# Kernel optimization log

Hardware: AMD Instinct MI355X
Metric: run time of the kernel (lower is better)

The kernel has to match this reference:

```python
import jax, jax.numpy as jnp
import numpy as np

N, E, IN_DIM, HID, HEADS, OUT_DIM, N_GRAPHS = 50000, 640000, 128, 64, 8, 2, 64
NEG_SLOPE = 0.2  # PyG GATConv default leaky_relu slope


def setup_inputs() -> dict:
    key = jax.random.key(0)
    ks = jax.random.split(key, 12)
    x = jax.random.normal(ks[0], (N, IN_DIM), jnp.float32)
    edge_index = jax.random.randint(ks[1], (2, E), 0, N, jnp.int32)
    batch = jnp.sort(jax.random.randint(ks[2], (N,), 0, N_GRAPHS, jnp.int32))
    def glorot(k, shape):
        fan_in = shape[0]
        return jax.random.normal(k, shape, jnp.float32) / np.sqrt(fan_in)
    return {
        "x": x,
        "W1": glorot(ks[3], (IN_DIM, HEADS * HID)),
        "att_src1": glorot(ks[4], (HEADS, HID)),
        "att_dst1": glorot(ks[5], (HEADS, HID)),
        "b1": jnp.zeros((HEADS * HID,), jnp.float32),
        "W2": glorot(ks[6], (HEADS * HID, HID)),
        "att_src2": glorot(ks[7], (1, HID)),
        "att_dst2": glorot(ks[8], (1, HID)),
        "b2": jnp.zeros((HID,), jnp.float32),
        "fc_w": glorot(ks[9], (HID, OUT_DIM)),
        "fc_b": jnp.zeros((OUT_DIM,), jnp.float32),
        "edge_index": edge_index,
        "batch": batch,
    }


def gat_layer(x, src, dst, W, a_src, a_dst, bias):
    # PyG GATConv: h = x @ W per head; alpha_e = LeakyReLU(a_src.h_src + a_dst.h_dst),
    # softmax over edges sharing the same dst, weighted scatter-sum, concat heads.
    H, C = a_src.shape
    h = (x @ W).reshape(-1, H, C)                       # [N, H, C]
    a_s = jnp.einsum('nhc,hc->nh', h, a_src)            # [N, H]
    a_d = jnp.einsum('nhc,hc->nh', h, a_dst)
    e = jax.nn.leaky_relu(a_s[src] + a_d[dst], NEG_SLOPE)  # [Etot, H]
    e_max = jax.ops.segment_max(e, dst, num_segments=N)
    e = jnp.exp(e - e_max[dst])
    denom = jax.ops.segment_sum(e, dst, num_segments=N)
    alpha = e / (denom[dst] + 1e-16)                    # edge softmax
    msg = h[src] * alpha[..., None]                     # [Etot, H, C]
    out = jax.ops.segment_sum(msg, dst, num_segments=N) # [N, H, C]
    return out.reshape(-1, H * C) + bias


def reference(x, W1, att_src1, att_dst1, b1, W2, att_src2, att_dst2, b2, fc_w, fc_b, edge_index, batch):
    # add self-loops (PyG GATConv default add_self_loops=True)
    loop = jnp.arange(N, dtype=edge_index.dtype)
    src = jnp.concatenate([edge_index[0], loop])
    dst = jnp.concatenate([edge_index[1], loop])

    h = gat_layer(x, src, dst, W1, att_src1, att_dst1, b1)   # [N, HEADS*HID]
    h = jax.nn.elu(h)
    # dropout is identity at eval
    h = gat_layer(h, src, dst, W2, att_src2, att_dst2, b2)   # [N, HID]
    h = jax.nn.elu(h)

    # global mean pool over graphs
    sums = jax.ops.segment_sum(h, batch, num_segments=N_GRAPHS)
    cnts = jax.ops.segment_sum(jnp.ones((N, 1), h.dtype), batch, num_segments=N_GRAPHS)
    pooled = sums / jnp.maximum(cnts, 1.0)                   # [G, HID]
    return pooled @ fc_w + fc_b                              # [G, OUT_DIM]
```

## Files before the change

### kernel.cpp

```cpp
#include <hip/hip_runtime.h>
#include <hip/hip_bf16.h>
#include <cstdint>
#include <cstddef>

#define N_NODES   50000
#define N_EDGES   640000
#define ETOT      (N_EDGES + N_NODES)
#define IN_DIM    128
#define HID       64
#define HEADS     8
#define F1        (HEADS * HID)
#define OUT_DIM   2
#define N_GRAPHS  64
#define NEG_SLOPE 0.2f
#define CAP       64

typedef __attribute__((ext_vector_type(8))) short s8v;
typedef __attribute__((ext_vector_type(4))) float f32x4;
typedef __attribute__((ext_vector_type(2))) float f32x2;
typedef unsigned char uchar;
typedef unsigned int  uint;
typedef unsigned long long u64;

__device__ __forceinline__ float leakyf(float x) { return x > 0.f ? x : NEG_SLOPE * x; }
__device__ __forceinline__ float eluf(float x)   { return x > 0.f ? x : __expf(x) - 1.f; }

__device__ __forceinline__ ushort f2bf(float f) {
    union { float f; uint32_t i; } c; c.f = f;
    uint32_t r = c.i + 0x7FFFu + ((c.i >> 16) & 1u);
    return (ushort)(r >> 16);
}
template<int SEL>
__device__ __forceinline__ float fp8f(uint w) {
    return __builtin_amdgcn_cvt_f32_fp8(w, SEL);
}
template<bool HI>
__device__ __forceinline__ f32x2 pk8(uint w) {
    return __builtin_amdgcn_cvt_pk_f32_fp8(w, HI);
}
__device__ __forceinline__ int orig64(int q) { return ((q & 3) << 4) | (q >> 2); }

#define W1_ITEMS  (F1 * IN_DIM)
#define W2_ITEMS  (HID * F1)
#define PM_ITEMS  (F1 + HID + HID * OUT_DIM)
#define PREP_ITEMS (ETOT + W1_ITEMS + W2_ITEMS + PM_ITEMS)

__global__ __launch_bounds__(256) void prep_fill(const int* __restrict__ srcI,
                                                 const int* __restrict__ dstI,
                                                 int* __restrict__ counts,
                                                 ushort* __restrict__ csrp,
                                                 const float* __restrict__ W1,
                                                 const float* __restrict__ W2,
                                                 const float* __restrict__ b1,
                                                 const float* __restrict__ b2,
                                                 const float* __restrict__ fcw,
                                                 ushort* __restrict__ W1T,
                                                 ushort* __restrict__ W2T,
                                                 float* __restrict__ b1p,
                                                 float* __restrict__ b2p,
                                                 float* __restrict__ fcwp) {
    int i = blockIdx.x * 256 + threadIdx.x;
    if (i < ETOT) {
        int s, d;
        if (i < N_EDGES) { s = srcI[i]; d = dstI[i]; }
        else             { s = d = i - N_EDGES; }
        int slot = atomicAdd(&counts[d], 1);
        if (slot < CAP) csrp[d * CAP + slot] = (ushort)s;
    } else if (i < ETOT + W1_ITEMS) {
        int idx = i - ETOT;
        int n = idx >> 7, k = idx & 127;
        W1T[idx] = f2bf(W1[(size_t)k * F1 + n]);
    } else if (i < ETOT + W1_ITEMS + W2_ITEMS) {
        int idx = i - ETOT - W1_ITEMS;
        int n = idx >> 9, kp = idx & 511;
        int ko = (kp & 448) | orig64(kp & 63);
        W2T[idx] = f2bf(W2[(size_t)ko * HID + n]);
    } else if (i < PREP_ITEMS) {
        int j = i - ETOT - W1_ITEMS - W2_ITEMS;
        if (j < F1) {
            b1p[j] = b1[(j & ~63) | orig64(j & 63)];
        } else if (j < F1 + HID) {
            int q = j - F1;
            b2p[q] = b2[orig64(q)];
        } else {
            int q = j - F1 - HID;
            int ch = q >> 1, o = q & 1;
            fcwp[q] = fcw[orig64(ch) * OUT_DIM + o];
        }
    }
}

template<int BM, int BN, int BK, int AH, bool AF32>
__global__ __launch_bounds__(256) void gemm_att(const void* __restrict__ Av,
                                                const ushort* __restrict__ BT,
                                                uchar* __restrict__ C8,
                                                int M, int N, int K,
                                                const float* __restrict__ att_s,
                                                const float* __restrict__ att_d,
                                                float* __restrict__ as_o,
                                                float* __restrict__ ad_o) {
    int nwg = gridDim.x;
    int q = nwg >> 3, r = nwg & 7;
    int xcd = blockIdx.x & 7, loc = blockIdx.x >> 3;
    int sid = (xcd < r) ? (xcd * (q + 1) + loc)
                        : (r * (q + 1) + (xcd - r) * q + loc);
    int ncb = N / BN;
    int bx = sid % ncb;
    int by = sid / ncb;

    __shared__ ushort As[BM * BK];
    __shared__ ushort Bs[BN * BK];
    const int t    = threadIdx.x;
    const int row0 = by * BM;
    const int col0 = bx * BN;
    const int lane = t & 63;
    const int wr   = t >> 6;
    constexpr int FR = BM / 64;

    f32x4 acc[FR][4];
    #pragma unroll
    for (int i = 0; i < FR; ++i)
        #pragma unroll
        for (int j = 0; j < 4; ++j)
            acc[i][j] = (f32x4){0.f, 0.f, 0.f, 0.f};

    constexpr int A_IT = BM * BK / 8 / 256;
    constexpr int B_IT = BN * BK / 8 / 256;

    for (int k0 = 0; k0 < K; k0 += BK) {
        #pragma unroll
        for (int i = 0; i < A_IT; ++i) {
            int ch  = t + 256 * i;
            int rr  = ch >> 3;
            int c16 = ch & 7;
            int gr = row0 + rr;
            uint4 v = make_uint4(0u, 0u, 0u, 0u);
            if constexpr (AF32) {
                const float* Af = (const float*)Av;
                if (gr < M) {
                    const float* pr = Af + (size_t)gr * K + k0 + c16 * 8;
                    float4 f0 = *reinterpret_cast<const float4*>(pr);
                    float4 f1 = *reinterpret_cast<const float4*>(pr + 4);
                    v.x = ((uint)f2bf(f0.y) << 16) | f2bf(f0.x);
                    v.y = ((uint)f2bf(f0.w) << 16) | f2bf(f0.z);
                    v.z = ((uint)f2bf(f1.y) << 16) | f2bf(f1.x);
                    v.w = ((uint)f2bf(f1.w) << 16) | f2bf(f1.z);
                }
            } else {
                const ushort* Ab = (const ushort*)Av;
                if (gr < M)
                    v = *reinterpret_cast<const uint4*>(Ab + (size_t)gr * K + k0 + c16 * 8);
            }
            int off = (ch * 16) ^ ((rr & 7) << 4);
            *reinterpret_cast<uint4*>(reinterpret_cast<char*>(As) + off) = v;
        }
        #pragma unroll
        for (int i = 0; i < B_IT; ++i) {
            int ch  = t + 256 * i;
            int rr  = ch >> 3;
            int c16 = ch & 7;
            uint4 v = *reinterpret_cast<const uint4*>(BT + (size_t)(col0 + rr) * K + k0 + c16 * 8);
            int off = (ch * 16) ^ ((rr & 7) << 4);
            *reinterpret_cast<uint4*>(reinterpret_cast<char*>(Bs) + off) = v;
        }
        __syncthreads();
        #pragma unroll
        for (int kk = 0; kk < BK; kk += 32) {
            s8v af[FR], bf[4];
            #pragma unroll
            for (int fr = 0; fr < FR; ++fr) {
                int rr  = wr * (FR * 16) + fr * 16 + (lane & 15);
                int off = (rr * (BK * 2) + kk * 2 + (lane >> 4) * 16) ^ ((rr & 7) << 4);
                af[fr] = *reinterpret_cast<const s8v*>(reinterpret_cast<const char*>(As) + off);
            }
            #pragma unroll
            for (int fc = 0; fc < 4; ++fc) {
                int rr  = fc * 16 + (lane & 15);
                int off = (rr * (BK * 2) + kk * 2 + (lane >> 4) * 16) ^ ((rr & 7) << 4);
                bf[fc] = *reinterpret_cast<const s8v*>(reinterpret_cast<const char*>(Bs) + off);
            }
            #pragma unroll
            for (int fr = 0; fr < FR; ++fr)
                #pragma unroll
                for (int fc = 0; fc < 4; ++fc)
                    acc[fr][fc] = __builtin_amdgcn_mfma_f32_16x16x32_bf16(af[fr], bf[fc], acc[fr][fc], 0, 0, 0);
        }
        __syncthreads();
    }

    float avs[4], avd[4];
    const float* asp = att_s + bx * BN;
    const float* adp = att_d + bx * BN;
    #pragma unroll
    for (int fc = 0; fc < 4; ++fc) {
        avs[fc] = asp[fc * 16 + (lane & 15)];
        avd[fc] = adp[fc * 16 + (lane & 15)];
    }

    #pragma unroll
    for (int fr = 0; fr < FR; ++fr) {
        #pragma unroll
        for (int j = 0; j < 4; ++j) {
            int row = row0 + wr * (FR * 16) + fr * 16 + (lane >> 4) * 4 + j;
            if (row < M) {
                uint pk = __builtin_amdgcn_cvt_pk_fp8_f32(acc[fr][0][j], acc[fr][1][j], 0u, false);
                pk = __builtin_amdgcn_cvt_pk_fp8_f32(acc[fr][2][j], acc[fr][3][j], pk, true);
                *reinterpret_cast<uint*>(C8 + (size_t)row * N + col0 + (lane & 15) * 4) = pk;
                float sv = 0.f, dv = 0.f;
                #pragma unroll
                for (int fc = 0; fc < 4; ++fc) {
                    float c = acc[fr][fc][j];
                    sv = fmaf(c, avs[fc], sv);
                    dv = fmaf(c, avd[fc], dv);
                }
                #pragma unroll
                for (int off = 1; off < 16; off <<= 1) {
                    sv += __shfl_xor(sv, off);
                    dv += __shfl_xor(dv, off);
                }
                if ((lane & 15) == 0) {
                    as_o[(size_t)row * AH + bx] = sv;
                    ad_o[(size_t)row * AH + bx] = dv;
                }
            }
        }
    }
}

__global__ __launch_bounds__(256) void gat_agg1(const uchar* __restrict__ h8,
                                                const float* __restrict__ as,
                                                const float* __restrict__ ad,
                                                const int* __restrict__ counts,
                                                const ushort* __restrict__ csrp,
                                                const float* __restrict__ b1p,
                                                ushort* __restrict__ z) {
    __shared__ float lds_w[4][HEADS][CAP + 1];
    int tid  = threadIdx.x;
    int wid  = tid >> 6;
    int dst  = (blockIdx.x * 256 + tid) >> 6;
    int lane = tid & 63;
    if (dst >= N_NODES) return;
    int cnt = min(counts[dst], CAP);
    int hd  = lane >> 3;

    int myidx = (lane < cnt) ? (int)csrp[(size_t)dst * CAP + lane] : 0;
    float4 a0 = *reinterpret_cast<const float4*>(as + (size_t)myidx * HEADS);
    float4 a1 = *reinterpret_cast<const float4*>(as + (size_t)myidx * HEADS + 4);
    float4 d0 = *reinterpret_cast<const float4*>(ad + (size_t)dst * HEADS);
    float4 d1 = *reinterpret_cast<const float4*>(ad + (size_t)dst * HEADS + 4);
    lds_w[wid][0][lane] = __expf(leakyf(a0.x + d0.x));
    lds_w[wid][1][lane] = __expf(leakyf(a0.y + d0.y));
    lds_w[wid][2][lane] = __expf(leakyf(a0.z + d0.z));
    lds_w[wid][3][lane] = __expf(leakyf(a0.w + d0.w));
    lds_w[wid][4][lane] = __expf(leakyf(a1.x + d1.x));
    lds_w[wid][5][lane] = __expf(leakyf(a1.y + d1.y));
    lds_w[wid][6][lane] = __expf(leakyf(a1.z + d1.z));
    lds_w[wid][7][lane] = __expf(leakyf(a1.w + d1.w));

    f32x2 acc2[4];
    acc2[0] = (f32x2){0.f, 0.f}; acc2[1] = (f32x2){0.f, 0.f};
    acc2[2] = (f32x2){0.f, 0.f}; acc2[3] = (f32x2){0.f, 0.f};
    float den = 0.f;
    const uchar* hb = h8 + (size_t)lane * 8;
    for (int j0 = 0; j0 < cnt; j0 += 4) {
        int n = cnt - j0;
        int s0 = 0, s1 = 0, s2 = 0, s3 = 0;
        u64 v0 = 0, v1 = 0, v2 = 0, v3 = 0;
        float w0 = 0.f, w1 = 0.f, w2 = 0.f, w3 = 0.f;
        s0 = __shfl(myidx, j0);
        v0 = __builtin_nontemporal_load(reinterpret_cast<const u64*>(hb + (size_t)s0 * F1));
        w0 = lds_w[wid][hd][j0];
        if (n > 1) {
            s1 = __shfl(myidx, j0 + 1);
            v1 = __builtin_nontemporal_load(reinterpret_cast<const u64*>(hb + (size_t)s1 * F1));
            w1 = lds_w[wid][hd][j0 + 1];
        }
        if (n > 2) {
            s2 = __shfl(myidx, j0 + 2);
            v2 = __builtin_nontemporal_load(reinterpret_cast<const u64*>(hb + (size_t)s2 * F1));
            w2 = lds_w[wid][hd][j0 + 2];
        }
        if (n > 3) {
            s3 = __shfl(myidx, j0 + 3);
            v3 = __builtin_nontemporal_load(reinterpret_cast<const u64*>(hb + (size_t)s3 * F1));
            w3 = lds_w[wid][hd][j0 + 3];
        }
        {
            f32x2 wv = (f32x2){w0, w0};
            den += w0;
            acc2[0] += pk8<false>((uint)v0) * wv;
            acc2[1] += pk8<true >((uint)v0) * wv;
            acc2[2] += pk8<false>((uint)(v0 >> 32)) * wv;
            acc2[3] += pk8<true >((uint)(v0 >> 32)) * wv;
        }
        if (n > 1) {
            f32x2 wv = (f32x2){w1, w1};
            den += w1;
            acc2[0] += pk8<false>((uint)v1) * wv;
            acc2[1] += pk8<true >((uint)v1) * wv;
            acc2[2] += pk8<false>((uint)(v1 >> 32)) * wv;
            acc2[3] += pk8<true >((uint)(v1 >> 32)) * wv;
        }
        if (n > 2) {
            f32x2 wv = (f32x2){w2, w2};
            den += w2;
            acc2[0] += pk8<false>((uint)v2) * wv;
            acc2[1] += pk8<true >((uint)v2) * wv;
            acc2[2] += pk8<false>((uint)(v2 >> 32)) * wv;
            acc2[3] += pk8<true >((uint)(v2 >> 32)) * wv;
        }
        if (n > 3) {
            f32x2 wv = (f32x2){w3, w3};
            den += w3;
            acc2[0] += pk8<false>((uint)v3) * wv;
            acc2[1] += pk8<true >((uint)v3) * wv;
            acc2[2] += pk8<false>((uint)(v3 >> 32)) * wv;
            acc2[3] += pk8<true >((uint)(v3 >> 32)) * wv;
        }
    }
    float inv = 1.f / (den + 1e-16f);
    s8v ov;
    #pragma unroll
    for (int c = 0; c < 8; ++c) {
        float v = acc2[c >> 1][c & 1] * inv + b1p[lane * 8 + c];
        ov[c] = (short)f2bf(eluf(v));
    }
    *reinterpret_cast<s8v*>(z + (size_t)dst * F1 + lane * 8) = ov;
}

__global__ __launch_bounds__(256) void gat_agg2(const uchar* __restrict__ h8,
                                                const float* __restrict__ as,
                                                const float* __restrict__ ad,
                                                const int* __restrict__ counts,
                                                const ushort* __restrict__ csrp,
                                                const float* __restrict__ b2p,
                                                float* __restrict__ z) {
    int dst  = (blockIdx.x * 256 + threadIdx.x) >> 6;
    int lane = threadIdx.x & 63;
    if (dst >= N_NODES) return;
    int cnt = min(counts[dst], CAP);
    float adv = ad[dst];

    int myidx = (lane < cnt) ? (int)csrp[(size_t)dst * CAP + lane] : 0;
    float wl  = (lane < cnt) ? __expf(leakyf(as[myidx] + adv)) : 0.f;
    float den = wl;
    #pragma unroll
    for (int off = 32; off > 0; off >>= 1) den += __shfl_xor(den, off);

    float acc = 0.f;
    for (int j0 = 0; j0 < cnt; j0 += 4) {
        int n = cnt - j0;
        int s0 = 0, s1 = 0, s2 = 0, s3 = 0;
        float w0 = 0.f, w1 = 0.f, w2 = 0.f, w3 = 0.f;
        uint b0 = 0, b1 = 0, b2 = 0, b3 = 0;
        s0 = __shfl(myidx, j0);     w0 = __shfl(wl, j0);
        b0 = h8[(size_t)s0 * HID + lane];
        if (n > 1) { s1 = __shfl(myidx, j0 + 1); w1 = __shfl(wl, j0 + 1); b1 = h8[(size_t)s1 * HID + lane]; }
        if (n > 2) { s2 = __shfl(myidx, j0 + 2); w2 = __shfl(wl, j0 + 2); b2 = h8[(size_t)s2 * HID + lane]; }
        if (n > 3) { s3 = __shfl(myidx, j0 + 3); w3 = __shfl(wl, j0 + 3); b3 = h8[(size_t)s3 * HID + lane]; }
        acc = fmaf(w0, fp8f<0>(b0), acc);
        if (n > 1) acc = fmaf(w1, fp8f<0>(b1), acc);
        if (n > 2) acc = fmaf(w2, fp8f<0>(b2), acc);
        if (n > 3) acc = fmaf(w3, fp8f<0>(b3), acc);
    }
    float v = acc / (den + 1e-16f) + b2p[lane];
    z[(size_t)dst * HID + lane] = eluf(v);
}

__global__ __launch_bounds__(512) void pool_fc(const float* __restrict__ z,
                                               const int* __restrict__ batch,
                                               const float* __restrict__ fcwp,
                                               const float* __restrict__ fc_b,
                                               float* __restrict__ out) {
    int g = blockIdx.x;
    int t = threadIdx.x, lane = t & 63, w = t >> 6;
    auto lb = [&](int key) {
        int lo = 0, hi = N_NODES;
        while (lo < hi) { int mid = (lo + hi) >> 1; if (batch[mid] < key) lo = mid + 1; else hi = mid; }
        return lo;
    };
    int lo = lb(g), hi = lb(g + 1);
    float a0 = 0.f, a1 = 0.f, a2 = 0.f, a3 = 0.f;
    for (int n0 = lo + (w << 2); n0 < hi; n0 += 32) {
        a0 += z[(size_t)n0 * HID + lane];
        if (n0 + 1 < hi) a1 += z[(size_t)(n0 + 1) * HID + lane];
        if (n0 + 2 < hi) a2 += z[(size_t)(n0 + 2) * HID + lane];
        if (n0 + 3 < hi) a3 += z[(size_t)(n0 + 3) * HID + lane];
    }
    float acc = (a0 + a1) + (a2 + a3);
    __shared__ float sh[8][HID];
    sh[w][lane] = acc;
    __syncthreads();
    if (w == 0) {
        float s = 0.f;
        #pragma unroll
        for (int i = 0; i < 8; ++i) s += sh[i][lane];
        float cntf = fmaxf((float)(hi - lo), 1.f);
        float mean = s / cntf;
        float p0 = mean * fcwp[lane * OUT_DIM + 0];
        float p1 = mean * fcwp[lane * OUT_DIM + 1];
        #pragma unroll
        for (int off = 32; off > 0; off >>= 1) {
            p0 += __shfl_xor(p0, off);
            p1 += __shfl_xor(p1, off);
        }
        if (lane == 0) {
            out[g * OUT_DIM + 0] = p0 + fc_b[0];
            out[g * OUT_DIM + 1] = p1 + fc_b[1];
        }
    }
}

extern "C" void kernel_launch(void* const* d_in, const int* in_sizes, int n_in,
                              void* d_out, int out_size, void* d_ws, size_t ws_size,
                              hipStream_t stream) {
    const float* x    = (const float*)d_in[0];
    const float* W1   = (const float*)d_in[1];
    const float* at_s1= (const float*)d_in[2];
    const float* at_d1= (const float*)d_in[3];
    const float* b1   = (const float*)d_in[4];
    const float* W2   = (const float*)d_in[5];
    const float* at_s2= (const float*)d_in[6];
    const float* at_d2= (const float*)d_in[7];
    const float* b2   = (const float*)d_in[8];
    const float* fcw  = (const float*)d_in[9];
    const float* fcb  = (const float*)d_in[10];
    const int*   ei   = (const int*)d_in[11];
    const int*   batch= (const int*)d_in[12];
    float* out = (float*)d_out;

    char* p = (char*)d_ws;
    auto alloc = [&](size_t bytes) {
        char* r = p;
        p += (bytes + 255) & ~size_t(255);
        return r;
    };
    int*    counts= (int*)alloc((size_t)N_NODES * 4);
    ushort* W1T   = (ushort*)alloc((size_t)F1 * IN_DIM * 2);
    ushort* W2T   = (ushort*)alloc((size_t)HID * F1 * 2);
    float*  b1p   = (float*)alloc((size_t)F1 * 4);
    float*  b2p   = (float*)alloc((size_t)HID * 4);
    float*  fcwp  = (float*)alloc((size_t)HID * OUT_DIM * 4);
    uchar*  h1    = (uchar*)alloc((size_t)N_NODES * F1);
    ushort* z1    = (ushort*)alloc((size_t)N_NODES * F1 * 2);
    uchar*  h2    = (uchar*)alloc((size_t)N_NODES * HID);
    float*  z2    = (float*)alloc((size_t)N_NODES * HID * 4);
    float*  as1   = (float*)alloc((size_t)N_NODES * HEADS * 4);
    float*  ad1   = (float*)alloc((size_t)N_NODES * HEADS * 4);
    float*  as2   = (float*)alloc((size_t)N_NODES * 4);
    float*  ad2   = (float*)alloc((size_t)N_NODES * 4);
    ushort* csrp  = (ushort*)alloc((size_t)N_NODES * CAP * 2);

    const int* srcI = ei;
    const int* dstI = ei + N_EDGES;

    (void)hipMemsetAsync(counts, 0, (size_t)N_NODES * 4, stream);

    prep_fill<<<(PREP_ITEMS + 255) / 256, 256, 0, stream>>>(
        srcI, dstI, counts, csrp, W1, W2, b1, b2, fcw, W1T, W2T, b1p, b2p, fcwp);

    int nwg1 = (F1 / 64) * ((N_NODES + 127) / 128);
    gemm_att<128, 64, 64, HEADS, true><<<nwg1, 256, 0, stream>>>(
        x, W1T, h1, N_NODES, F1, IN_DIM, at_s1, at_d1, as1, ad1);
    gat_agg1<<<(N_NODES + 3) / 4, 256, 0, stream>>>(h1, as1, ad1, counts, csrp, b1p, z1);

    int nwg2 = 1 * ((N_NODES + 127) / 128);
    gemm_att<128, 64, 64, 1, false><<<nwg2, 256, 0, stream>>>(
        z1, W2T, h2, N_NODES, HID, F1, at_s2, at_d2, as2, ad2);
    gat_agg2<<<(N_NODES + 3) / 4, 256, 0, stream>>>(h2, as2, ad2, counts, csrp, b2p, z2);

    pool_fc<<<N_GRAPHS, 512, 0, stream>>>(z2, batch, fcwp, fcb, out);
}
```

Measured before the change: 308.5 us.

## Fuse mean-pool into second aggregation via atomics; retile layer-2 GEMM; drop nontemporal loads

The second GAT aggregation now reduces its ELU outputs per graph inside each block and atomically adds them into a small per-graph sum buffer. This removes the 12.8MB z2 write and the re-read by the pooling kernel, and a tiny single-block kernel then applies the mean and the FC layer. The psum zeroing is folded into the existing memset. The layer-2 GEMM tile shrinks from 128 to 64 rows to get more workgroups, and the layer-1 gather loads switch from nontemporal to normal cached loads. Atomic accumulation makes the float summation order nondeterministic.

```diff
diff --git a/kernel.cpp b/kernel.cpp
--- a/kernel.cpp
+++ b/kernel.cpp
@@ -268,21 +268,21 @@
         u64 v0 = 0, v1 = 0, v2 = 0, v3 = 0;
         float w0 = 0.f, w1 = 0.f, w2 = 0.f, w3 = 0.f;
         s0 = __shfl(myidx, j0);
-        v0 = __builtin_nontemporal_load(reinterpret_cast<const u64*>(hb + (size_t)s0 * F1));
+        v0 = *reinterpret_cast<const u64*>(hb + (size_t)s0 * F1);
         w0 = lds_w[wid][hd][j0];
         if (n > 1) {
             s1 = __shfl(myidx, j0 + 1);
-            v1 = __builtin_nontemporal_load(reinterpret_cast<const u64*>(hb + (size_t)s1 * F1));
+            v1 = *reinterpret_cast<const u64*>(hb + (size_t)s1 * F1);
             w1 = lds_w[wid][hd][j0 + 1];
         }
         if (n > 2) {
             s2 = __shfl(myidx, j0 + 2);
-            v2 = __builtin_nontemporal_load(reinterpret_cast<const u64*>(hb + (size_t)s2 * F1));
+            v2 = *reinterpret_cast<const u64*>(hb + (size_t)s2 * F1);
             w2 = lds_w[wid][hd][j0 + 2];
         }
         if (n > 3) {
             s3 = __shfl(myidx, j0 + 3);
-            v3 = __builtin_nontemporal_load(reinterpret_cast<const u64*>(hb + (size_t)s3 * F1));
+            v3 = *reinterpret_cast<const u64*>(hb + (size_t)s3 * F1);
             w3 = lds_w[wid][hd][j0 + 3];
         }
         {
@@ -334,10 +334,14 @@
                                                 const int* __restrict__ counts,
                                                 const ushort* __restrict__ csrp,
                                                 const float* __restrict__ b2p,
-                                                float* __restrict__ z) {
-    int dst  = (blockIdx.x * 256 + threadIdx.x) >> 6;
-    int lane = threadIdx.x & 63;
-    if (dst >= N_NODES) return;
+                                                const int* __restrict__ batch,
+                                                float* __restrict__ psum) {
+    __shared__ float shz[4][HID];
+    __shared__ int   shg[4];
+    int tid  = threadIdx.x;
+    int wid  = tid >> 6;
+    int dst  = (blockIdx.x * 256 + tid) >> 6;
+    int lane = tid & 63;
     int cnt = min(counts[dst], CAP);
     float adv = ad[dst];
 
@@ -363,52 +367,43 @@
         if (n > 2) acc = fmaf(w2, fp8f<0>(b2), acc);
         if (n > 3) acc = fmaf(w3, fp8f<0>(b3), acc);
     }
-    float v = acc / (den + 1e-16f) + b2p[lane];
-    z[(size_t)dst * HID + lane] = eluf(v);
-}
-
-__global__ __launch_bounds__(512) void pool_fc(const float* __restrict__ z,
-                                               const int* __restrict__ batch,
-                                               const float* __restrict__ fcwp,
-                                               const float* __restrict__ fc_b,
-                                               float* __restrict__ out) {
-    int g = blockIdx.x;
-    int t = threadIdx.x, lane = t & 63, w = t >> 6;
+    float v = eluf(acc / (den + 1e-16f) + b2p[lane]);
+
+    shz[wid][lane] = v;
+    if (lane == 0) shg[wid] = batch[dst];
+    __syncthreads();
+    if (wid == 0) {
+        float s = shz[0][lane];
+        int   g = shg[0];
+        #pragma unroll
+        for (int i = 1; i < 4; ++i) {
+            if (shg[i] == g) s += shz[i][lane];
+            else {
+                atomicAdd(&psum[(size_t)g * HID + lane], s);
+                s = shz[i][lane]; g = shg[i];
+            }
+        }
+        atomicAdd(&psum[(size_t)g * HID + lane], s);
+    }
+}
+
+__global__ __launch_bounds__(128) void final_fc(const float* __restrict__ psum,
+                                                const int* __restrict__ batch,
+                                                const float* __restrict__ fcwp,
+                                                const float* __restrict__ fc_b,
+                                                float* __restrict__ out) {
+    int t = threadIdx.x;
+    int g = t >> 1, o = t & 1;
     auto lb = [&](int key) {
         int lo = 0, hi = N_NODES;
         while (lo < hi) { int mid = (lo + hi) >> 1; if (batch[mid] < key) lo = mid + 1; else hi = mid; }
         return lo;
     };
-    int lo = lb(g), hi = lb(g + 1);
-    float a0 = 0.f, a1 = 0.f, a2 = 0.f, a3 = 0.f;
-    for (int n0 = lo + (w << 2); n0 < hi; n0 += 32) {
-        a0 += z[(size_t)n0 * HID + lane];
-        if (n0 + 1 < hi) a1 += z[(size_t)(n0 + 1) * HID + lane];
-        if (n0 + 2 < hi) a2 += z[(size_t)(n0 + 2) * HID + lane];
-        if (n0 + 3 < hi) a3 += z[(size_t)(n0 + 3) * HID + lane];
-    }
-    float acc = (a0 + a1) + (a2 + a3);
-    __shared__ float sh[8][HID];
-    sh[w][lane] = acc;
-    __syncthreads();
-    if (w == 0) {
-        float s = 0.f;
-        #pragma unroll
-        for (int i = 0; i < 8; ++i) s += sh[i][lane];
-        float cntf = fmaxf((float)(hi - lo), 1.f);
-        float mean = s / cntf;
-        float p0 = mean * fcwp[lane * OUT_DIM + 0];
-        float p1 = mean * fcwp[lane * OUT_DIM + 1];
-        #pragma unroll
-        for (int off = 32; off > 0; off >>= 1) {
-            p0 += __shfl_xor(p0, off);
-            p1 += __shfl_xor(p1, off);
-        }
-        if (lane == 0) {
-            out[g * OUT_DIM + 0] = p0 + fc_b[0];
-            out[g * OUT_DIM + 1] = p1 + fc_b[1];
-        }
-    }
+    float cnt = fmaxf((float)(lb(g + 1) - lb(g)), 1.0f);
+    float s = 0.f;
+    for (int c = 0; c < HID; ++c)
+        s += psum[(size_t)g * HID + c] * fcwp[c * OUT_DIM + o];
+    out[g * OUT_DIM + o] = s / cnt + fc_b[o];
 }
 
 extern "C" void kernel_launch(void* const* d_in, const int* in_sizes, int n_in,
@@ -436,6 +431,9 @@
         return r;
     };
     int*    counts= (int*)alloc((size_t)N_NODES * 4);
+    float*  psum  = (float*)alloc((size_t)N_GRAPHS * HID * 4);
+    size_t zero_bytes = (size_t)(p - (char*)counts);
+
     ushort* W1T   = (ushort*)alloc((size_t)F1 * IN_DIM * 2);
     ushort* W2T   = (ushort*)alloc((size_t)HID * F1 * 2);
     float*  b1p   = (float*)alloc((size_t)F1 * 4);
@@ -444,7 +442,6 @@
     uchar*  h1    = (uchar*)alloc((size_t)N_NODES * F1);
     ushort* z1    = (ushort*)alloc((size_t)N_NODES * F1 * 2);
     uchar*  h2    = (uchar*)alloc((size_t)N_NODES * HID);
-    float*  z2    = (float*)alloc((size_t)N_NODES * HID * 4);
     float*  as1   = (float*)alloc((size_t)N_NODES * HEADS * 4);
     float*  ad1   = (float*)alloc((size_t)N_NODES * HEADS * 4);
     float*  as2   = (float*)alloc((size_t)N_NODES * 4);
@@ -454,7 +451,7 @@
     const int* srcI = ei;
     const int* dstI = ei + N_EDGES;
 
-    (void)hipMemsetAsync(counts, 0, (size_t)N_NODES * 4, stream);
+    (void)hipMemsetAsync(counts, 0, zero_bytes, stream);
 
     prep_fill<<<(PREP_ITEMS + 255) / 256, 256, 0, stream>>>(
         srcI, dstI, counts, csrp, W1, W2, b1, b2, fcw, W1T, W2T, b1p, b2p, fcwp);
@@ -464,10 +461,11 @@
         x, W1T, h1, N_NODES, F1, IN_DIM, at_s1, at_d1, as1, ad1);
     gat_agg1<<<(N_NODES + 3) / 4, 256, 0, stream>>>(h1, as1, ad1, counts, csrp, b1p, z1);
 
-    int nwg2 = 1 * ((N_NODES + 127) / 128);
-    gemm_att<128, 64, 64, 1, false><<<nwg2, 256, 0, stream>>>(
+    int nwg2 = 1 * ((N_NODES + 63) / 64);
+    gemm_att<64, 64, 64, 1, false><<<nwg2, 256, 0, stream>>>(
         z1, W2T, h2, N_NODES, HID, F1, at_s2, at_d2, as2, ad2);
-    gat_agg2<<<(N_NODES + 3) / 4, 256, 0, stream>>>(h2, as2, ad2, counts, csrp, b2p, z2);
-
-    pool_fc<<<N_GRAPHS, 512, 0, stream>>>(z2, batch, fcwp, fcb, out);
-}
+
+    gat_agg2<<<N_NODES / 4, 256, 0, stream>>>(h2, as2, ad2, counts, csrp, b2p, batch, psum);
+
+    final_fc<<<1, 128, 0, stream>>>(psum, batch, fcwp, fcb, out);
+}
```

Result: faster. 278.0 us (-9.9%).
